# Optimization experiments

Measured on AMD Instinct MI355X. Metric: run time of the kernel, lower is better.

## Reference

```python
import jax, jax.numpy as jnp
import numpy as np

N_NODES = 500_000
N_FEAT = 125          # embedding dim; cat with pos(3) -> 128
HIDDEN = 128
OUT_DIM = 64
N_TYPES = 100
N_GRAPHS = 4096


def setup_inputs() -> dict:
    key = jax.random.key(0)
    ks = jax.random.split(key, 10)
    pos = jax.random.normal(ks[0], (N_NODES, 3), dtype=jnp.float32)
    z = jax.random.randint(ks[1], (N_NODES,), 0, N_TYPES)
    batch = jnp.sort(jax.random.randint(ks[2], (N_NODES,), 0, N_GRAPHS))
    emb = jax.random.normal(ks[3], (N_TYPES, N_FEAT), dtype=jnp.float32)
    s1 = 1.0 / np.sqrt(N_FEAT + 3)
    s2 = 1.0 / np.sqrt(HIDDEN)
    W1 = jax.random.normal(ks[4], (N_FEAT + 3, HIDDEN), dtype=jnp.float32) * s1
    b1 = jnp.zeros((HIDDEN,), dtype=jnp.float32)
    W2 = jax.random.normal(ks[5], (HIDDEN, HIDDEN), dtype=jnp.float32) * s2
    b2 = jnp.zeros((HIDDEN,), dtype=jnp.float32)
    W3 = jax.random.normal(ks[6], (HIDDEN, OUT_DIM), dtype=jnp.float32) * s2
    b3 = jnp.zeros((OUT_DIM,), dtype=jnp.float32)
    return {"pos": pos, "z": z, "batch": batch, "emb": emb,
            "W1": W1, "b1": b1, "W2": W2, "b2": b2, "W3": W3, "b3": b3}


def reference(pos, z, batch, emb, W1, b1, W2, b2, W3, b3):
    # embed node types and concat with 3D positions  -> [N, 128]
    x = jnp.concatenate([pos, emb[z]], axis=-1)
    # two equivariant-transformer layers (per-node transform) + relu
    x = jax.nn.relu(x @ W1 + b1)   # [N, H]
    x = jax.nn.relu(x @ W2 + b2)   # [N, H]
    # output head
    x = x @ W3 + b3                # [N, O]
    # global mean pool per graph
    s = jax.ops.segment_sum(x, batch, num_segments=N_GRAPHS)                    # [G, O]
    cnt = jax.ops.segment_sum(jnp.ones((x.shape[0], 1), x.dtype), batch,
                              num_segments=N_GRAPHS)                            # [G, 1]
    return s / jnp.maximum(cnt, 1.0)
```

## Files before the change

kernel.cpp:

```cpp
#include <hip/hip_runtime.h>
#include <hip/hip_bf16.h>

#define N_NODES 500000
#define N_FEAT 125
#define HID 128
#define OUTD 64
#define N_GRAPHS 4096
#define N_TYPES 100
#define WTILE 32
#define NBLOCKS 256
#define NTHREADS 512
#define NWAVES 8
#define WPAD 136
#define OPADF 68
#define NSLOTS 40

typedef float f32x4 __attribute__((ext_vector_type(4)));
typedef short s16x8 __attribute__((ext_vector_type(8)));

#define OFF_W2 0
#define OFF_W3 (OFF_W2 + HID * WPAD * 2)
#define OFF_B2 (OFF_W3 + OUTD * WPAD * 2)
#define OFF_T  (OFF_B2 + HID * 4)
#define OFF_SCR (OFF_T + N_TYPES * WPAD * 2)
#define SCR_BYTES (WTILE * WPAD * 2)
#define OFF_SLOT (OFF_SCR + NWAVES * SCR_BYTES)
#define OFF_CNT (OFF_SLOT + NSLOTS * OUTD * 4)
#define OFF_IDS (OFF_CNT + NSLOTS * 4)
#define LDS_BYTES (OFF_IDS + NWAVES * WTILE * 4)

__device__ __forceinline__ unsigned short f2bf(float f) {
  union { float f; unsigned u; } v; v.f = f;
  unsigned r = v.u + 0x7FFFu + ((v.u >> 16) & 1u);
  return (unsigned short)(r >> 16);
}
__device__ __forceinline__ float bf2f(unsigned short u) {
  union { unsigned u; float f; } v; v.u = ((unsigned)u) << 16;
  return v.f;
}
__device__ __forceinline__ unsigned pk2bf(float a, float b) {
  __hip_bfloat162 h = __float22bfloat162_rn(float2{a, b});
  union { __hip_bfloat162 h; unsigned u; } v; v.h = h;
  return v.u;
}

__device__ __forceinline__ void wavefence() {
  __builtin_amdgcn_sched_barrier(0);
  __builtin_amdgcn_wave_barrier();
  __builtin_amdgcn_sched_barrier(0);
}

extern "C" __global__ void __launch_bounds__(NTHREADS, 2)
gnn_all(const float* __restrict__ pos, const int* __restrict__ z,
        const int* __restrict__ batch, const float* __restrict__ emb,
        const float* __restrict__ W1, const float* __restrict__ b1,
        const float* __restrict__ W2, const float* __restrict__ b2,
        const float* __restrict__ W3, const float* __restrict__ b3,
        float* __restrict__ out)
{
  extern __shared__ char lds[];
  unsigned short* w2t = (unsigned short*)(lds + OFF_W2);
  unsigned short* w3t = (unsigned short*)(lds + OFF_W3);
  float* bias2 = (float*)(lds + OFF_B2);
  unsigned short* Tl = (unsigned short*)(lds + OFF_T);
  unsigned short* w1t = (unsigned short*)(lds + OFF_SCR);
  float* slotsum = (float*)(lds + OFF_SLOT);
  int* slotcnt = (int*)(lds + OFF_CNT);

  const int t = threadIdx.x, b = blockIdx.x;
  const int wave = t >> 6, lane = t & 63, quad = lane >> 4, l15 = lane & 15;

  const int tlo = 61 * b + (b < 9 ? b : 9);
  const int ntl = 61 + (b < 9 ? 1 : 0);
  const int start_node = tlo * WTILE;
  const int end_node = start_node + ntl * WTILE;

  for (int i = t; i < HID * HID; i += NTHREADS) {
    int k = i >> 7, n = i & 127;
    w2t[n * WPAD + k] = f2bf(W2[i]);
  }
  for (int i = t; i < HID * OUTD; i += NTHREADS) {
    int k = i >> 6, n = i & 63;
    w3t[n * WPAD + k] = f2bf(W3[i]);
  }
  for (int i = t; i < HID * HID; i += NTHREADS) {
    int k = i >> 7, j = i & 127;
    w1t[j * WPAD + k] = (k < N_FEAT) ? f2bf(W1[(3 + k) * HID + j]) : (unsigned short)0;
  }
  if (t < HID) bias2[t] = b2[t];

  for (int i = t; i < NSLOTS * OUTD; i += NTHREADS) slotsum[i] = 0.f;
  if (t < NSLOTS) slotcnt[t] = 0;

  const int slot_base = batch[start_node];
  const int prev_g = (b == 0) ? -1 : batch[start_node - 1];
  const int own_hi = batch[end_node - 1];
  int n_ext = 0;
  if (end_node < N_NODES) {
    while (end_node + WTILE * n_ext < N_NODES &&
           batch[end_node + WTILE * n_ext] == own_hi) ++n_ext;
  }

  float w1r[3][4][8];
  #pragma unroll
  for (int c = 0; c < 3; ++c)
    #pragma unroll
    for (int k = 0; k < 4; ++k)
      #pragma unroll
      for (int j = 0; j < 8; ++j)
        w1r[c][k][j] = W1[c * HID + k * 32 + quad * 8 + j];
  const float b3l = b3[lane];

  __syncthreads();

  {
    const int jt = wave;
    s16x8 afr[4];
    #pragma unroll
    for (int kf = 0; kf < 4; ++kf)
      afr[kf] = *(const s16x8*)(w1t + (jt * 16 + l15) * WPAD + kf * 32 + quad * 8);

    const int j0 = jt * 16 + quad * 4;
    const f32x4 b1v = *(const f32x4*)&b1[j0];

    for (int gt = 0; gt < 7; ++gt) {
      const int g = gt * 16 + l15;
      const int gg = (g < N_TYPES) ? g : (N_TYPES - 1);
      const float* erow = emb + gg * N_FEAT;
      f32x4 acc = {};
      #pragma unroll
      for (int kf = 0; kf < 4; ++kf) {
        s16x8 bf;
        #pragma unroll
        for (int u = 0; u < 8; ++u) {
          const int k = kf * 32 + quad * 8 + u;
          float v = (k < N_FEAT) ? erow[k] : 0.f;
          bf[u] = (short)f2bf(v);
        }
        acc = __builtin_amdgcn_mfma_f32_16x16x32_bf16(afr[kf], bf, acc, 0, 0, 0);
      }
      if (g < N_TYPES) {
        unsigned lo = pk2bf(acc[0] + b1v[0], acc[1] + b1v[1]);
        unsigned hi = pk2bf(acc[2] + b1v[2], acc[3] + b1v[3]);
        *(uint2*)(Tl + g * WPAD + j0) = uint2{lo, hi};
      }
    }
  }

  unsigned short* xs = (unsigned short*)(lds + OFF_SCR + wave * SCR_BYTES);
  float* xo = (float*)xs;
  int* ids = (int*)(lds + OFF_IDS) + wave * WTILE;

  __syncthreads();

  const int ntot = ntl + n_ext;
  for (int j = wave; j < ntot; j += NWAVES) {
    const int base = start_node + j * WTILE;

    if (lane < WTILE) ids[lane] = batch[base + lane];

    s16x8 a[2][4];
    #pragma unroll
    for (int m = 0; m < 2; ++m) {
      const int node = base + m * 16 + l15;
      const int zi = z[node];
      const float px = pos[node * 3], py = pos[node * 3 + 1], pz = pos[node * 3 + 2];
      const unsigned short* Tr = Tl + zi * WPAD;
      #pragma unroll
      for (int k = 0; k < 4; ++k) {
        s16x8 tf = *(const s16x8*)(Tr + k * 32 + quad * 8);
        s16x8 fr;
        #pragma unroll
        for (int jj = 0; jj < 8; jj += 2) {
          float v0 = bf2f((unsigned short)tf[jj])
                   + px * w1r[0][k][jj] + py * w1r[1][k][jj] + pz * w1r[2][k][jj];
          float v1 = bf2f((unsigned short)tf[jj + 1])
                   + px * w1r[0][k][jj + 1] + py * w1r[1][k][jj + 1] + pz * w1r[2][k][jj + 1];
          ((unsigned*)&fr)[jj >> 1] = pk2bf(fmaxf(v0, 0.f), fmaxf(v1, 0.f));
        }
        a[m][k] = fr;
      }
    }

    f32x4 acc[8][2] = {};
    #pragma unroll
    for (int oi = 0; oi < 8; ++oi)
      #pragma unroll
      for (int k = 0; k < 4; ++k) {
        s16x8 w = *(const s16x8*)(w2t + (oi * 16 + l15) * WPAD + k * 32 + quad * 8);
        acc[oi][0] = __builtin_amdgcn_mfma_f32_16x16x32_bf16(w, a[0][k], acc[oi][0], 0, 0, 0);
        acc[oi][1] = __builtin_amdgcn_mfma_f32_16x16x32_bf16(w, a[1][k], acc[oi][1], 0, 0, 0);
      }
    #pragma unroll
    for (int oi = 0; oi < 8; ++oi) {
      const int f0 = oi * 16 + quad * 4;
      f32x4 bv = *(const f32x4*)(bias2 + f0);
      #pragma unroll
      for (int m = 0; m < 2; ++m) {
        unsigned lo = pk2bf(fmaxf(acc[oi][m][0] + bv[0], 0.f),
                            fmaxf(acc[oi][m][1] + bv[1], 0.f));
        unsigned hi = pk2bf(fmaxf(acc[oi][m][2] + bv[2], 0.f),
                            fmaxf(acc[oi][m][3] + bv[3], 0.f));
        *(uint2*)(xs + (m * 16 + l15) * WPAD + f0) = uint2{lo, hi};
      }
    }
    wavefence();
    #pragma unroll
    for (int m = 0; m < 2; ++m)
      #pragma unroll
      for (int k = 0; k < 4; ++k)
        a[m][k] = *(const s16x8*)(xs + (m * 16 + l15) * WPAD + k * 32 + quad * 8);
    wavefence();

    f32x4 acc3[4][2] = {};
    #pragma unroll
    for (int oi = 0; oi < 4; ++oi)
      #pragma unroll
      for (int k = 0; k < 4; ++k) {
        s16x8 w = *(const s16x8*)(w3t + (oi * 16 + l15) * WPAD + k * 32 + quad * 8);
        acc3[oi][0] = __builtin_amdgcn_mfma_f32_16x16x32_bf16(w, a[0][k], acc3[oi][0], 0, 0, 0);
        acc3[oi][1] = __builtin_amdgcn_mfma_f32_16x16x32_bf16(w, a[1][k], acc3[oi][1], 0, 0, 0);
      }
    #pragma unroll
    for (int oi = 0; oi < 4; ++oi)
      #pragma unroll
      for (int m = 0; m < 2; ++m)
        *(f32x4*)(xo + (m * 16 + l15) * OPADF + oi * 16 + quad * 4) = acc3[oi][m];
    wavefence();

    {
      int cur = ids[0];
      float run = 0.f; int rc = 0;
      #pragma unroll 1
      for (int n = 0; n < WTILE; ++n) {
        int bb2 = ids[n];
        if (bb2 != cur) {
          if (cur != prev_g && cur <= own_hi) {
            atomicAdd(&slotsum[(cur - slot_base) * OUTD + lane], run);
            if (lane == 0) atomicAdd(&slotcnt[cur - slot_base], rc);
          }
          run = 0.f; rc = 0; cur = bb2;
        }
        run += xo[n * OPADF + lane]; rc++;
      }
      if (cur != prev_g && cur <= own_hi) {
        atomicAdd(&slotsum[(cur - slot_base) * OUTD + lane], run);
        if (lane == 0) atomicAdd(&slotcnt[cur - slot_base], rc);
      }
    }
    wavefence();
  }

  __syncthreads();

  const int own_lo = slot_base + (slot_base == prev_g ? 1 : 0);
  for (int g = own_lo + wave; g <= own_hi; g += NWAVES) {
    int s = g - slot_base;
    float sum = slotsum[s * OUTD + lane];
    int c = slotcnt[s];
    out[g * OUTD + lane] = (c > 0) ? (sum / (float)c + b3l) : 0.f;
  }
  const int next_g = (end_node < N_NODES) ? batch[end_node] : N_GRAPHS;
  for (int g = own_hi + 1 + wave; g < next_g; g += NWAVES)
    out[g * OUTD + lane] = 0.f;
  if (b == 0)
    for (int g = wave; g < slot_base; g += NWAVES)
      out[g * OUTD + lane] = 0.f;
}

extern "C" void kernel_launch(void* const* d_in, const int* in_sizes, int n_in,
                              void* d_out, int out_size, void* d_ws, size_t ws_size,
                              hipStream_t stream) {
  const float* pos  = (const float*)d_in[0];
  const int*   z    = (const int*)d_in[1];
  const int*   batch= (const int*)d_in[2];
  const float* emb  = (const float*)d_in[3];
  const float* W1   = (const float*)d_in[4];
  const float* b1   = (const float*)d_in[5];
  const float* W2   = (const float*)d_in[6];
  const float* b2   = (const float*)d_in[7];
  const float* W3   = (const float*)d_in[8];
  const float* b3   = (const float*)d_in[9];

  hipFuncSetAttribute((const void*)gnn_all,
                      hipFuncAttributeMaxDynamicSharedMemorySize, LDS_BYTES);

  hipLaunchKernelGGL(gnn_all, dim3(NBLOCKS), dim3(NTHREADS), LDS_BYTES, stream,
                     pos, z, batch, emb, W1, b1, W2, b2, W3, b3, (float*)d_out);
}
```

Measured before the change: 161.3 us.

## Stage embeddings in LDS, ballot-probe batch extent, and pack first-layer math

Several changes to the prologue and the per-node layer-1 path. The embedding table is staged into padded LDS as fp32 and read with vector loads. The W1 fragments are loaded straight from global memory into registers instead of going through an LDS transpose. The serial tail-extension scan over batch is replaced by a 12-lane ballot probe. The per-node position FMA, ReLU and bias add use packed two-wide float ops, aiming at v_pk_fma_f32. The intent is to cut prologue latency and VALU instruction count, at the cost of extra register pressure and uncoalesced strided global reads for W1.

Result: faster. 151.1 us (-6.3%).

```diff
diff --git a/kernel.cpp b/kernel.cpp
--- a/kernel.cpp
+++ b/kernel.cpp
@@ -14,8 +14,10 @@
 #define WPAD 136
 #define OPADF 68
 #define NSLOTS 40
+#define EPAD 132
 
 typedef float f32x4 __attribute__((ext_vector_type(4)));
+typedef float f32x2 __attribute__((ext_vector_type(2)));
 typedef short s16x8 __attribute__((ext_vector_type(8)));
 
 #define OFF_W2 0
@@ -34,14 +36,15 @@
   unsigned r = v.u + 0x7FFFu + ((v.u >> 16) & 1u);
   return (unsigned short)(r >> 16);
 }
-__device__ __forceinline__ float bf2f(unsigned short u) {
-  union { unsigned u; float f; } v; v.u = ((unsigned)u) << 16;
-  return v.f;
-}
 __device__ __forceinline__ unsigned pk2bf(float a, float b) {
   __hip_bfloat162 h = __float22bfloat162_rn(float2{a, b});
   union { __hip_bfloat162 h; unsigned u; } v; v.h = h;
   return v.u;
+}
+__device__ __forceinline__ f32x2 unpk_bf2(unsigned u) {
+  union { unsigned u; float f; } lo, hi;
+  lo.u = u << 16; hi.u = u & 0xffff0000u;
+  return (f32x2){lo.f, hi.f};
 }
 
 __device__ __forceinline__ void wavefence() {
@@ -63,7 +66,7 @@
   unsigned short* w3t = (unsigned short*)(lds + OFF_W3);
   float* bias2 = (float*)(lds + OFF_B2);
   unsigned short* Tl = (unsigned short*)(lds + OFF_T);
-  unsigned short* w1t = (unsigned short*)(lds + OFF_SCR);
+  float* embs = (float*)(lds + OFF_SCR);
   float* slotsum = (float*)(lds + OFF_SLOT);
   int* slotcnt = (int*)(lds + OFF_CNT);
 
@@ -83,9 +86,9 @@
     int k = i >> 6, n = i & 63;
     w3t[n * WPAD + k] = f2bf(W3[i]);
   }
-  for (int i = t; i < HID * HID; i += NTHREADS) {
-    int k = i >> 7, j = i & 127;
-    w1t[j * WPAD + k] = (k < N_FEAT) ? f2bf(W1[(3 + k) * HID + j]) : (unsigned short)0;
+  for (int i = t; i < N_TYPES * EPAD; i += NTHREADS) {
+    int g = i / EPAD, k = i - g * EPAD;
+    embs[i] = (k < N_FEAT) ? emb[g * N_FEAT + k] : 0.f;
   }
   if (t < HID) bias2[t] = b2[t];
 
@@ -97,46 +100,65 @@
   const int own_hi = batch[end_node - 1];
   int n_ext = 0;
   if (end_node < N_NODES) {
-    while (end_node + WTILE * n_ext < N_NODES &&
-           batch[end_node + WTILE * n_ext] == own_hi) ++n_ext;
-  }
-
-  float w1r[3][4][8];
+    int probe = -1;
+    if (lane < 12 && end_node + lane * WTILE < N_NODES)
+      probe = batch[end_node + lane * WTILE];
+    unsigned long long m = __ballot(probe == own_hi);
+    n_ext = (int)__builtin_ctzll(~m);
+    if (n_ext == 12) {
+      while (end_node + WTILE * n_ext < N_NODES &&
+             batch[end_node + WTILE * n_ext] == own_hi) ++n_ext;
+    }
+  }
+
+  f32x2 w1r2[3][4][4];
   #pragma unroll
   for (int c = 0; c < 3; ++c)
     #pragma unroll
     for (int k = 0; k < 4; ++k)
       #pragma unroll
-      for (int j = 0; j < 8; ++j)
-        w1r[c][k][j] = W1[c * HID + k * 32 + quad * 8 + j];
+      for (int p = 0; p < 4; ++p)
+        w1r2[c][k][p] = *(const f32x2*)&W1[c * HID + k * 32 + quad * 8 + 2 * p];
   const float b3l = b3[lane];
 
-  __syncthreads();
-
+  s16x8 afr[4];
   {
     const int jt = wave;
-    s16x8 afr[4];
-    #pragma unroll
-    for (int kf = 0; kf < 4; ++kf)
-      afr[kf] = *(const s16x8*)(w1t + (jt * 16 + l15) * WPAD + kf * 32 + quad * 8);
-
+    #pragma unroll
+    for (int kf = 0; kf < 4; ++kf) {
+      s16x8 fr;
+      #pragma unroll
+      for (int u = 0; u < 8; ++u) {
+        const int k = kf * 32 + quad * 8 + u;
+        float v = (k < N_FEAT) ? W1[(3 + k) * HID + jt * 16 + l15] : 0.f;
+        fr[u] = (short)f2bf(v);
+      }
+      afr[kf] = fr;
+    }
+  }
+
+  __syncthreads();
+
+  {
+    const int jt = wave;
     const int j0 = jt * 16 + quad * 4;
     const f32x4 b1v = *(const f32x4*)&b1[j0];
 
     for (int gt = 0; gt < 7; ++gt) {
       const int g = gt * 16 + l15;
       const int gg = (g < N_TYPES) ? g : (N_TYPES - 1);
-      const float* erow = emb + gg * N_FEAT;
+      const float* erow = embs + gg * EPAD;
       f32x4 acc = {};
       #pragma unroll
       for (int kf = 0; kf < 4; ++kf) {
+        const int k0 = kf * 32 + quad * 8;
+        f32x4 e0 = *(const f32x4*)(erow + k0);
+        f32x4 e1 = *(const f32x4*)(erow + k0 + 4);
         s16x8 bf;
-        #pragma unroll
-        for (int u = 0; u < 8; ++u) {
-          const int k = kf * 32 + quad * 8 + u;
-          float v = (k < N_FEAT) ? erow[k] : 0.f;
-          bf[u] = (short)f2bf(v);
-        }
+        ((unsigned*)&bf)[0] = pk2bf(e0[0], e0[1]);
+        ((unsigned*)&bf)[1] = pk2bf(e0[2], e0[3]);
+        ((unsigned*)&bf)[2] = pk2bf(e1[0], e1[1]);
+        ((unsigned*)&bf)[3] = pk2bf(e1[2], e1[3]);
         acc = __builtin_amdgcn_mfma_f32_16x16x32_bf16(afr[kf], bf, acc, 0, 0, 0);
       }
       if (g < N_TYPES) {
@@ -164,19 +186,22 @@
     for (int m = 0; m < 2; ++m) {
       const int node = base + m * 16 + l15;
       const int zi = z[node];
-      const float px = pos[node * 3], py = pos[node * 3 + 1], pz = pos[node * 3 + 2];
+      const f32x2 px2 = {pos[node * 3], pos[node * 3]};
+      const f32x2 py2 = {pos[node * 3 + 1], pos[node * 3 + 1]};
+      const f32x2 pz2 = {pos[node * 3 + 2], pos[node * 3 + 2]};
       const unsigned short* Tr = Tl + zi * WPAD;
       #pragma unroll
       for (int k = 0; k < 4; ++k) {
         s16x8 tf = *(const s16x8*)(Tr + k * 32 + quad * 8);
         s16x8 fr;
         #pragma unroll
-        for (int jj = 0; jj < 8; jj += 2) {
-          float v0 = bf2f((unsigned short)tf[jj])
-                   + px * w1r[0][k][jj] + py * w1r[1][k][jj] + pz * w1r[2][k][jj];
-          float v1 = bf2f((unsigned short)tf[jj + 1])
-                   + px * w1r[0][k][jj + 1] + py * w1r[1][k][jj + 1] + pz * w1r[2][k][jj + 1];
-          ((unsigned*)&fr)[jj >> 1] = pk2bf(fmaxf(v0, 0.f), fmaxf(v1, 0.f));
+        for (int p = 0; p < 4; ++p) {
+          f32x2 tv = unpk_bf2(((const unsigned*)&tf)[p]);
+          tv = __builtin_elementwise_fma(px2, w1r2[0][k][p], tv);
+          tv = __builtin_elementwise_fma(py2, w1r2[1][k][p], tv);
+          tv = __builtin_elementwise_fma(pz2, w1r2[2][k][p], tv);
+          tv = __builtin_elementwise_max(tv, (f32x2){0.f, 0.f});
+          ((unsigned*)&fr)[p] = pk2bf(tv[0], tv[1]);
         }
         a[m][k] = fr;
       }
@@ -197,10 +222,10 @@
       f32x4 bv = *(const f32x4*)(bias2 + f0);
       #pragma unroll
       for (int m = 0; m < 2; ++m) {
-        unsigned lo = pk2bf(fmaxf(acc[oi][m][0] + bv[0], 0.f),
-                            fmaxf(acc[oi][m][1] + bv[1], 0.f));
-        unsigned hi = pk2bf(fmaxf(acc[oi][m][2] + bv[2], 0.f),
-                            fmaxf(acc[oi][m][3] + bv[3], 0.f));
+        f32x4 s = acc[oi][m] + bv;
+        s = __builtin_elementwise_max(s, (f32x4){0.f, 0.f, 0.f, 0.f});
+        unsigned lo = pk2bf(s[0], s[1]);
+        unsigned hi = pk2bf(s[2], s[3]);
         *(uint2*)(xs + (m * 16 + l15) * WPAD + f0) = uint2{lo, hi};
       }
     }
```
